# Kernel tuning notes

Hardware: AMD Instinct MI355X
Metric: run time of the kernel (lower is better)

The kernel has to match this reference:

```python
import jax, jax.numpy as jnp
import numpy as np

VOCAB, DIM, HEADS, LAYERS = 32000, 1024, 16, 2
B, S = 2, 1024
HD = DIM // HEADS


def rmsnorm(x, g, eps=1e-6):
    return x * jax.lax.rsqrt(jnp.mean(x * x, axis=-1, keepdims=True) + eps) * g


def setup_inputs() -> dict:
    key = jax.random.key(0)
    ks = jax.random.split(key, 20)
    s = 0.02
    d = {
        "text_ids": jax.random.randint(ks[0], (B, S), 0, VOCAB),
        "embed": jax.random.normal(ks[1], (VOCAB, DIM), jnp.float32) * s,
        "g1": jnp.ones((LAYERS, DIM), jnp.float32),
        "wq": jax.random.normal(ks[2], (LAYERS, DIM, DIM), jnp.float32) * s,
        "bq": jnp.zeros((LAYERS, DIM), jnp.float32),
        "wk": jax.random.normal(ks[3], (LAYERS, DIM, DIM), jnp.float32) * s,
        "bk": jnp.zeros((LAYERS, DIM), jnp.float32),
        "wv": jax.random.normal(ks[4], (LAYERS, DIM, DIM), jnp.float32) * s,
        "bv": jnp.zeros((LAYERS, DIM), jnp.float32),
        "wo": jax.random.normal(ks[5], (LAYERS, DIM, DIM), jnp.float32) * s,
        "bo": jnp.zeros((LAYERS, DIM), jnp.float32),
        "g2": jnp.ones((LAYERS, DIM), jnp.float32),
        "w1": jax.random.normal(ks[6], (LAYERS, DIM, 4 * DIM), jnp.float32) * s,
        "b1": jnp.zeros((LAYERS, 4 * DIM), jnp.float32),
        "w2": jax.random.normal(ks[7], (LAYERS, 4 * DIM, DIM), jnp.float32) * s,
        "b2": jnp.zeros((LAYERS, DIM), jnp.float32),
        "gf": jnp.ones((DIM,), jnp.float32),
        "head_w": jax.random.normal(ks[8], (DIM, VOCAB), jnp.float32) * s,
        "head_b": jnp.zeros((VOCAB,), jnp.float32),
    }
    return d


def reference(text_ids, embed, g1, wq, bq, wk, bk, wv, bv, wo, bo,
              g2, w1, b1, w2, b2, gf, head_w, head_b):
    b, s = text_ids.shape
    x = embed[text_ids]                                   # [B,S,D]
    causal = jnp.tril(jnp.ones((s, s), dtype=bool))        # [S,S]
    scale = 1.0 / jnp.sqrt(jnp.asarray(HD, x.dtype))
    for l in range(LAYERS):
        # attention sublayer: x = x + attn(norm1(x))
        h = rmsnorm(x, g1[l])
        q = (h @ wq[l] + bq[l]).reshape(b, s, HEADS, HD)
        k = (h @ wk[l] + bk[l]).reshape(b, s, HEADS, HD)
        v = (h @ wv[l] + bv[l]).reshape(b, s, HEADS, HD)
        scores = jnp.einsum("bqhd,bkhd->bhqk", q, k) * scale
        scores = jnp.where(causal, scores, jnp.asarray(-1e30, scores.dtype))
        a = jax.nn.softmax(scores, axis=-1)
        o = jnp.einsum("bhqk,bkhd->bqhd", a, v).reshape(b, s, DIM)
        x = x + (o @ wo[l] + bo[l])
        # FFN sublayer: x = x + ffn(norm2(x)), SiLU MLP (MoE unused in source forward)
        h2 = rmsnorm(x, g2[l])
        x = x + (jax.nn.silu(h2 @ w1[l] + b1[l]) @ w2[l] + b2[l])
    x = rmsnorm(x, gf)
    return x.astype(jnp.float32) @ head_w + head_b         # [B,S,VOCAB]
```

## Files before the change

kernel.cpp:

```cpp
#include <hip/hip_runtime.h>

#define LAYERS 2
#define DIM 1024
#define HEADS 16
#define HD 64
#define BATCH 2
#define SEQ 1024
#define ROWS (BATCH * SEQ)
#define FFN (4 * DIM)
#define VOCAB 32000
#define QKVN (3 * DIM)

typedef unsigned short u16;
typedef short vshort8 __attribute__((ext_vector_type(8)));
typedef float f32x4 __attribute__((ext_vector_type(4)));

#define VMCNT(n) asm volatile("s_waitcnt vmcnt(" #n ")" ::: "memory")

__device__ __forceinline__ u16 f2bf(float f) {
  union { float f; unsigned u; } x{f};
  unsigned r = (x.u + 0x7fffu + ((x.u >> 16) & 1u)) >> 16;
  return (u16)r;
}

__device__ __forceinline__ void gll16(const void* g, u16* l) {
  __builtin_amdgcn_global_load_lds(
      (const __attribute__((address_space(1))) void*)g,
      (__attribute__((address_space(3))) void*)l, 16, 0, 0);
}

__device__ __forceinline__ int xcd_swizzle(int orig, int nwg) {
  int q = nwg >> 3, r = nwg & 7;
  int xcd = orig & 7;
  int base = (xcd < r) ? xcd * (q + 1) : r * (q + 1) + (xcd - r) * q;
  return base + (orig >> 3);
}

__global__ __launch_bounds__(256) void transpose_sq_kernel(
    const float* __restrict__ wq, const float* __restrict__ wk,
    const float* __restrict__ wv, const float* __restrict__ wo,
    u16* __restrict__ wqkvT, u16* __restrict__ woT) {
  __shared__ float tile[32][33];
  int z = blockIdx.z, l = z >> 2, wsel = z & 3;
  const float* src =
      (wsel == 0 ? wq : wsel == 1 ? wk : wsel == 2 ? wv : wo) +
      (size_t)l * DIM * DIM;
  u16* dst = (wsel < 3)
                 ? wqkvT + (size_t)l * QKVN * DIM + (size_t)wsel * DIM * DIM
                 : woT + (size_t)l * DIM * DIM;
  int c0 = blockIdx.x * 32, r0 = blockIdx.y * 32;
  int tx = threadIdx.x, ty = threadIdx.y;
#pragma unroll
  for (int i = 0; i < 4; i++)
    tile[ty + i * 8][tx] = src[(size_t)(r0 + ty + i * 8) * DIM + c0 + tx];
  __syncthreads();
#pragma unroll
  for (int i = 0; i < 4; i++)
    dst[(size_t)(c0 + ty + i * 8) * DIM + r0 + tx] = f2bf(tile[tx][ty + i * 8]);
}

template <int R, int C>
__global__ __launch_bounds__(256) void transpose_rc_kernel(
    const float* __restrict__ srcb, u16* __restrict__ dstb) {
  __shared__ float tile[32][33];
  int l = blockIdx.z;
  const float* src = srcb + (size_t)l * R * C;
  u16* dst = dstb + (size_t)l * R * C;
  int c0 = blockIdx.x * 32, r0 = blockIdx.y * 32;
  int tx = threadIdx.x, ty = threadIdx.y;
#pragma unroll
  for (int i = 0; i < 4; i++)
    tile[ty + i * 8][tx] = src[(size_t)(r0 + ty + i * 8) * C + c0 + tx];
  __syncthreads();
#pragma unroll
  for (int i = 0; i < 4; i++)
    dst[(size_t)(c0 + ty + i * 8) * R + r0 + tx] = f2bf(tile[tx][ty + i * 8]);
}

__global__ __launch_bounds__(256) void pack_qkv_bias(
    const float* __restrict__ bq, const float* __restrict__ bk,
    const float* __restrict__ bv, float* __restrict__ o) {
  int l = blockIdx.y;
  int t = blockIdx.x * 256 + threadIdx.x;
  float v;
  if (t < DIM) v = bq[l * DIM + t];
  else if (t < 2 * DIM) v = bk[l * DIM + t - DIM];
  else v = bv[l * DIM + t - 2 * DIM];
  o[(size_t)l * QKVN + t] = v;
}

__global__ __launch_bounds__(256) void embed_gather(
    const int* __restrict__ ids, const float* __restrict__ emb,
    float* __restrict__ x) {
  int row = blockIdx.x;
  int id = ids[row];
  const float4* s = (const float4*)(emb + (size_t)id * DIM);
  float4* d = (float4*)(x + (size_t)row * DIM);
  d[threadIdx.x] = s[threadIdx.x];
}

__global__ __launch_bounds__(256) void rmsnorm_kernel(
    const float* __restrict__ x, const float* __restrict__ g,
    u16* __restrict__ out) {
  int row = blockIdx.x;
  int t = threadIdx.x;
  const float4* xr = (const float4*)(x + (size_t)row * DIM);
  float4 v = xr[t];
  float ss = v.x * v.x + v.y * v.y + v.z * v.z + v.w * v.w;
  for (int off = 32; off > 0; off >>= 1) ss += __shfl_down(ss, off);
  __shared__ float part[4];
  if ((t & 63) == 0) part[t >> 6] = ss;
  __syncthreads();
  float tot = part[0] + part[1] + part[2] + part[3];
  float r = rsqrtf(tot / (float)DIM + 1e-6f);
  float4 gv = ((const float4*)g)[t];
  ushort4 o;
  o.x = f2bf(v.x * r * gv.x);
  o.y = f2bf(v.y * r * gv.y);
  o.z = f2bf(v.z * r * gv.z);
  o.w = f2bf(v.w * r * gv.w);
  *(ushort4*)(out + (size_t)row * DIM + t * 4) = o;
}

__global__ __launch_bounds__(256) void addnorm_kernel(
    float* __restrict__ x, const float* __restrict__ P0,
    const float* __restrict__ P1, const float* __restrict__ bias,
    const float* __restrict__ g, u16* __restrict__ h) {
  int row = blockIdx.x;
  int t = threadIdx.x;
  float4 v = ((const float4*)(x + (size_t)row * DIM))[t];
  float4 a = ((const float4*)(P0 + (size_t)row * DIM))[t];
  float4 b = ((const float4*)(P1 + (size_t)row * DIM))[t];
  float4 c = ((const float4*)bias)[t];
  v.x += a.x + b.x + c.x;
  v.y += a.y + b.y + c.y;
  v.z += a.z + b.z + c.z;
  v.w += a.w + b.w + c.w;
  ((float4*)(x + (size_t)row * DIM))[t] = v;
  float ss = v.x * v.x + v.y * v.y + v.z * v.z + v.w * v.w;
  for (int off = 32; off > 0; off >>= 1) ss += __shfl_down(ss, off);
  __shared__ float part[4];
  if ((t & 63) == 0) part[t >> 6] = ss;
  __syncthreads();
  float tot = part[0] + part[1] + part[2] + part[3];
  float r = rsqrtf(tot / (float)DIM + 1e-6f);
  float4 gv = ((const float4*)g)[t];
  ushort4 o;
  o.x = f2bf(v.x * r * gv.x);
  o.y = f2bf(v.y * r * gv.y);
  o.z = f2bf(v.z * r * gv.z);
  o.w = f2bf(v.w * r * gv.w);
  *(ushort4*)(h + (size_t)row * DIM + t * 4) = o;
}

template <int OUTBF, int SILU, int SPLITK, int MFAST, int VT>
__global__ __launch_bounds__(256, 2) void gemm128_kernel(
    const u16* __restrict__ A, const u16* __restrict__ Wt,
    const float* __restrict__ bias, void* __restrict__ outv,
    float* __restrict__ pout1, u16* __restrict__ vt2, int M, int N, int K) {
  __shared__ u16 As[2][128 * 64];
  __shared__ u16 Bs[2][128 * 64];
  int nm = M >> 7, nn = N >> 7, nwg = nm * nn;
  int wg = xcd_swizzle(blockIdx.x, SPLITK ? nwg * 2 : nwg);
  int ks = 0;
  if (SPLITK) { ks = wg >= nwg; wg -= ks * nwg; }
  int mi, ni;
  if (MFAST) { mi = wg % nm; ni = wg / nm; }
  else       { ni = wg % nn; mi = wg / nn; }
  int m0 = mi << 7, n0 = ni << 7;
  int kb = SPLITK ? ks * (K >> 1) : 0;
  int NTt = (SPLITK ? (K >> 1) : K) >> 6;
  int tid = threadIdx.x, wave = tid >> 6, lane = tid & 63;
  int wr = wave >> 1, wc = wave & 1;
  int r16 = lane & 15, g4 = lane >> 4;
  int lrow = lane >> 3, lslot = lane & 7;

  f32x4 acc[4][4] = {};

  auto stage = [&](int buf, int kt) {
#pragma unroll
    for (int i = 0; i < 4; i++) {
      int s = wave * 4 + i;
      int row = s * 8 + lrow;
      int slot = lslot ^ (row & 7);
      gll16(A + (size_t)(m0 + row) * K + kb + kt * 64 + slot * 8,
            &As[buf][s * 512 + lane * 8]);
    }
#pragma unroll
    for (int i = 0; i < 4; i++) {
      int s = wave * 4 + i;
      int row = s * 8 + lrow;
      int slot = lslot ^ (row & 7);
      gll16(Wt + (size_t)(n0 + row) * K + kb + kt * 64 + slot * 8,
            &Bs[buf][s * 512 + lane * 8]);
    }
  };

  stage(0, 0);
  VMCNT(0);
  __builtin_amdgcn_s_barrier();

  for (int t = 0; t < NTt; t++) {
    int cur = t & 1;
    if (t + 1 < NTt) stage(cur ^ 1, t + 1);
#pragma unroll
    for (int kk = 0; kk < 2; kk++) {
      vshort8 af[4], bf[4];
#pragma unroll
      for (int m = 0; m < 4; m++) {
        int r = wr * 64 + m * 16 + r16;
        int slot = (kk * 4 + g4) ^ (r & 7);
        af[m] = *(const vshort8*)&As[cur][r * 64 + slot * 8];
      }
#pragma unroll
      for (int n = 0; n < 4; n++) {
        int c = wc * 64 + n * 16 + r16;
        int slot = (kk * 4 + g4) ^ (c & 7);
        bf[n] = *(const vshort8*)&Bs[cur][c * 64 + slot * 8];
      }
#pragma unroll
      for (int m = 0; m < 4; m++)
#pragma unroll
        for (int n = 0; n < 4; n++)
          acc[m][n] = __builtin_amdgcn_mfma_f32_16x16x32_bf16(af[m], bf[n],
                                                              acc[m][n], 0, 0, 0);
    }
    VMCNT(0);
    __builtin_amdgcn_s_barrier();
  }

  if (SPLITK) {
    float* P = ks ? pout1 : (float*)outv;
#pragma unroll
    for (int m = 0; m < 4; m++) {
      int rowb = m0 + wr * 64 + m * 16 + g4 * 4;
#pragma unroll
      for (int n = 0; n < 4; n++) {
        int col = n0 + wc * 64 + n * 16 + r16;
#pragma unroll
        for (int j = 0; j < 4; j++)
          P[(size_t)(rowb + j) * N + col] = acc[m][n][j];
      }
    }
  } else {
#pragma unroll
    for (int m = 0; m < 4; m++) {
      int rowb = m0 + wr * 64 + m * 16 + g4 * 4;
#pragma unroll
      for (int n = 0; n < 4; n++) {
        int col = n0 + wc * 64 + n * 16 + r16;
        float b = bias[col];
        u16 ov[4];
#pragma unroll
        for (int j = 0; j < 4; j++) {
          float v = acc[m][n][j] + b;
          if (SILU) v = v / (1.f + __expf(-v));
          if (OUTBF) ov[j] = f2bf(v);
          else ((float*)outv)[(size_t)(rowb + j) * N + col] = v;
        }
        if (OUTBF) {
          if (VT && col >= 2 * DIM) {
            int dv = col - 2 * DIM;
            int hh = dv >> 6, dd = dv & 63;
            int bb = rowb >> 10, s = rowb & 1023;
            ushort4 o4{ov[0], ov[1], ov[2], ov[3]};
            *(ushort4*)&vt2[((((size_t)(bb * 16 + hh) * (SEQ / 8) + (s >> 3)) * 64 +
                              dd) * 8) + (s & 7)] = o4;
          } else {
#pragma unroll
            for (int j = 0; j < 4; j++)
              ((u16*)outv)[(size_t)(rowb + j) * N + col] = ov[j];
          }
        }
      }
    }
  }
}

__global__ __launch_bounds__(512, 2) void gemm256p_kernel(
    const u16* __restrict__ A, const u16* __restrict__ Wt,
    const float* __restrict__ bias, float* __restrict__ out,
    int M, int N, int K) {
  __shared__ u16 As[2][256 * 64];
  __shared__ u16 Bs[2][256 * 64];
  int nn = N >> 8;
  int wg = xcd_swizzle(blockIdx.x, nn * 2);
  int ni = wg >> 1, mhalf = wg & 1;
  int n0 = ni << 8;
  int tid = threadIdx.x, w = tid >> 6, lane = tid & 63;
  int wr = w >> 2, wc = w & 3;
  int r16 = lane & 15, g4 = lane >> 4;
  int srow8 = lane >> 3, sslot = lane & 7;
  const int NTK = 16;
  const int NGT = 64;

  f32x4 acc[8][4] = {};

  auto stageA = [&](int buf, int mb, int kt, int hb, int j) {
    int chunk = j * 8 + w;
    int row = hb * 128 + chunk * 8 + srow8;
    int slot = sslot ^ (row & 7);
    gll16(A + (size_t)(mb + row) * K + kt * 64 + slot * 8,
          &As[buf][hb * 8192 + chunk * 512 + lane * 8]);
  };
  auto stageB = [&](int buf, int kt, int hb, int j) {
    int chunk = j * 8 + w;
    int row = hb * 128 + chunk * 8 + srow8;
    int slot = sslot ^ (row & 7);
    gll16(Wt + (size_t)(n0 + row) * K + kt * 64 + slot * 8,
          &Bs[buf][hb * 8192 + chunk * 512 + lane * 8]);
  };
  auto readA = [&](int buf, int mf, int kk) -> vshort8 {
    int row = mf * 32 + wr * 16 + r16;
    int slot = (kk * 4 + g4) ^ (row & 7);
    return *(const vshort8*)&As[buf][row * 64 + slot * 8];
  };
  auto readB = [&](int buf, int nf, int kk) -> vshort8 {
    int row = nf * 64 + wc * 16 + r16;
    int slot = (kk * 4 + g4) ^ (row & 7);
    return *(const vshort8*)&Bs[buf][row * 64 + slot * 8];
  };

  int mb0 = (mhalf * 4) << 8;
  stageA(0, mb0, 0, 0, 0); stageA(0, mb0, 0, 0, 1);
  stageB(0, 0, 0, 0);      stageB(0, 0, 0, 1);
  stageB(0, 0, 1, 0);      stageB(0, 0, 1, 1);
  stageA(0, mb0, 0, 1, 0); stageA(0, mb0, 0, 1, 1);
  VMCNT(2);
  __builtin_amdgcn_s_barrier();

  vshort8 af[4][2], bf0[2][2], bf1[2][2];

  for (int ti = 0; ti < 4; ti++) {
    int m0 = (mhalf * 4 + ti) << 8;
    for (int tt = 0; tt < NTK; tt++) {
      int gt = ti * NTK + tt;
      int cur = gt & 1, nxt = cur ^ 1;
      int gt1 = gt + 1;
      bool hn = gt1 < NGT;
      int kt1 = gt1 & (NTK - 1);
      int mb1 = (mhalf * 4 + (gt1 >> 4)) << 8;
      if (hn) {
        stageA(nxt, mb1, kt1, 0, 0); stageA(nxt, mb1, kt1, 0, 1);
        stageB(nxt, kt1, 0, 0);      stageB(nxt, kt1, 0, 1);
        stageB(nxt, kt1, 1, 0);      stageB(nxt, kt1, 1, 1);
      }
#pragma unroll
      for (int m = 0; m < 4; m++)
#pragma unroll
        for (int kk = 0; kk < 2; kk++) af[m][kk] = readA(cur, m, kk);
#pragma unroll
      for (int n = 0; n < 2; n++)
#pragma unroll
        for (int kk = 0; kk < 2; kk++) {
          bf0[n][kk] = readB(cur, n, kk);
          bf1[n][kk] = readB(cur, 2 + n, kk);
        }
      __builtin_amdgcn_s_barrier();
      __builtin_amdgcn_s_setprio(1);
#pragma unroll
      for (int m = 0; m < 4; m++)
#pragma unroll
        for (int n = 0; n < 2; n++)
#pragma unroll
          for (int kk = 0; kk < 2; kk++) {
            acc[m][n] = __builtin_amdgcn_mfma_f32_16x16x32_bf16(
                af[m][kk], bf0[n][kk], acc[m][n], 0, 0, 0);
            acc[m][n + 2] = __builtin_amdgcn_mfma_f32_16x16x32_bf16(
                af[m][kk], bf1[n][kk], acc[m][n + 2], 0, 0, 0);
          }
      __builtin_amdgcn_s_setprio(0);
      VMCNT(6);
      __builtin_amdgcn_s_barrier();
      if (hn) { stageA(nxt, mb1, kt1, 1, 0); stageA(nxt, mb1, kt1, 1, 1); }
#pragma unroll
      for (int m = 0; m < 4; m++)
#pragma unroll
        for (int kk = 0; kk < 2; kk++) af[m][kk] = readA(cur, 4 + m, kk);
      __builtin_amdgcn_s_barrier();
      __builtin_amdgcn_s_setprio(1);
#pragma unroll
      for (int m = 0; m < 4; m++)
#pragma unroll
        for (int n = 0; n < 2; n++)
#pragma unroll
          for (int kk = 0; kk < 2; kk++) {
            acc[m + 4][n] = __builtin_amdgcn_mfma_f32_16x16x32_bf16(
                af[m][kk], bf0[n][kk], acc[m + 4][n], 0, 0, 0);
            acc[m + 4][n + 2] = __builtin_amdgcn_mfma_f32_16x16x32_bf16(
                af[m][kk], bf1[n][kk], acc[m + 4][n + 2], 0, 0, 0);
          }
      __builtin_amdgcn_s_setprio(0);
      VMCNT(2);
      __builtin_amdgcn_s_barrier();
    }
#pragma unroll
    for (int mf = 0; mf < 8; mf++) {
      int rowb = m0 + mf * 32 + wr * 16 + g4 * 4;
#pragma unroll
      for (int nf = 0; nf < 4; nf++) {
        int col = n0 + nf * 64 + wc * 16 + r16;
        float b = bias[col];
#pragma unroll
        for (int j = 0; j < 4; j++)
          out[(size_t)(rowb + j) * N + col] = acc[mf][nf][j] + b;
      }
    }
#pragma unroll
    for (int mf = 0; mf < 8; mf++)
#pragma unroll
      for (int nf = 0; nf < 4; nf++) acc[mf][nf] = f32x4{0.f, 0.f, 0.f, 0.f};
  }
}

__global__ __launch_bounds__(256) void attn_kernel(const u16* __restrict__ qkv,
                                                   const u16* __restrict__ vt2,
                                                   u16* __restrict__ o) {
  __shared__ u16 Ks[2][32 * 64];
  __shared__ u16 pl[4][16 * 40];
  int qblk = blockIdx.x, bh = blockIdx.y;
  int b = bh >> 4, h = bh & 15;
  int tid = threadIdx.x, w = tid >> 6, lane = tid & 63;
  int r16 = lane & 15, g4 = lane >> 4;
  int q0 = qblk * 64 + w * 16;

  const u16* qrow = qkv + ((size_t)(b * SEQ) + q0 + r16) * QKVN + h * HD;
  vshort8 aq0 = *(const vshort8*)(qrow + g4 * 8);
  vshort8 aq1 = *(const vshort8*)(qrow + 32 + g4 * 8);

  float mrun[4], lrun[4];
  f32x4 accO[4];
#pragma unroll
  for (int j = 0; j < 4; j++) { mrun[j] = -1e30f; lrun[j] = 0.f; }
#pragma unroll
  for (int d = 0; d < 4; d++) accO[d] = f32x4{0.f, 0.f, 0.f, 0.f};

  int nkvT = qblk * 2 + 2;
  auto stageK = [&](int buf, int kt) {
    int row = tid >> 3;
    int slot = (tid & 7) ^ (row & 7);
    gll16(qkv + ((size_t)(b * SEQ) + kt * 32 + row) * QKVN + DIM + h * HD + slot * 8,
          &Ks[buf][w * 512 + lane * 8]);
  };
  stageK(0, 0);
  __syncthreads();
  int buf = 0;
  for (int kt = 0; kt < nkvT; kt++) {
    int kv0 = kt * 32;
    if (kt + 1 < nkvT) stageK(buf ^ 1, kt + 1);
    if (kv0 <= q0 + 15) {
      int row0 = r16, row1 = 16 + r16;
      vshort8 bk00 = *(const vshort8*)&Ks[buf][row0 * 64 + ((0 + g4) ^ (row0 & 7)) * 8];
      vshort8 bk01 = *(const vshort8*)&Ks[buf][row0 * 64 + ((4 + g4) ^ (row0 & 7)) * 8];
      vshort8 bk10 = *(const vshort8*)&Ks[buf][row1 * 64 + ((0 + g4) ^ (row1 & 7)) * 8];
      vshort8 bk11 = *(const vshort8*)&Ks[buf][row1 * 64 + ((4 + g4) ^ (row1 & 7)) * 8];
      f32x4 s0 = {}, s1 = {};
      s0 = __builtin_amdgcn_mfma_f32_16x16x32_bf16(aq0, bk00, s0, 0, 0, 0);
      s0 = __builtin_amdgcn_mfma_f32_16x16x32_bf16(aq1, bk01, s0, 0, 0, 0);
      s1 = __builtin_amdgcn_mfma_f32_16x16x32_bf16(aq0, bk10, s1, 0, 0, 0);
      s1 = __builtin_amdgcn_mfma_f32_16x16x32_bf16(aq1, bk11, s1, 0, 0, 0);

#pragma unroll
      for (int j = 0; j < 4; j++) {
        int qg = q0 + g4 * 4 + j;
        float x0 = s0[j] * 0.125f;
        float x1 = s1[j] * 0.125f;
        if (kv0 + r16 > qg) x0 = -1e30f;
        if (kv0 + 16 + r16 > qg) x1 = -1e30f;
        float mx = fmaxf(x0, x1);
#pragma unroll
        for (int mm = 1; mm < 16; mm <<= 1) mx = fmaxf(mx, __shfl_xor(mx, mm));
        float mnew = fmaxf(mrun[j], mx);
        float alpha = __expf(mrun[j] - mnew);
        float p0 = __expf(x0 - mnew);
        float p1 = __expf(x1 - mnew);
        float rs = p0 + p1;
#pragma unroll
        for (int mm = 1; mm < 16; mm <<= 1) rs += __shfl_xor(rs, mm);
        lrun[j] = lrun[j] * alpha + rs;
        mrun[j] = mnew;
#pragma unroll
        for (int d = 0; d < 4; d++) accO[d][j] *= alpha;
        pl[w][(g4 * 4 + j) * 40 + r16] = f2bf(p0);
        pl[w][(g4 * 4 + j) * 40 + 16 + r16] = f2bf(p1);
      }
      asm volatile("s_waitcnt lgkmcnt(0)" ::: "memory");
      vshort8 ap = *(const vshort8*)&pl[w][r16 * 40 + g4 * 8];
      const u16* vbase = vt2 + (((size_t)bh * (SEQ / 8) + (kv0 >> 3) + g4) * 64) * 8;
#pragma unroll
      for (int d = 0; d < 4; d++) {
        vshort8 bv = *(const vshort8*)(vbase + (size_t)(d * 16 + r16) * 8);
        accO[d] = __builtin_amdgcn_mfma_f32_16x16x32_bf16(ap, bv, accO[d], 0, 0, 0);
      }
    }
    __syncthreads();
    buf ^= 1;
  }

#pragma unroll
  for (int j = 0; j < 4; j++) {
    float inv = 1.f / lrun[j];
    int row = q0 + g4 * 4 + j;
#pragma unroll
    for (int d = 0; d < 4; d++)
      o[((size_t)(b * SEQ) + row) * DIM + h * HD + d * 16 + r16] =
          f2bf(accO[d][j] * inv);
  }
}

extern "C" void kernel_launch(void* const* d_in, const int* in_sizes, int n_in,
                              void* d_out, int out_size, void* d_ws,
                              size_t ws_size, hipStream_t stream) {
  const int* ids = (const int*)d_in[0];
  const float* emb = (const float*)d_in[1];
  const float* g1 = (const float*)d_in[2];
  const float* wq = (const float*)d_in[3];
  const float* bq = (const float*)d_in[4];
  const float* wk = (const float*)d_in[5];
  const float* bk = (const float*)d_in[6];
  const float* wv = (const float*)d_in[7];
  const float* bv = (const float*)d_in[8];
  const float* wo = (const float*)d_in[9];
  const float* bo = (const float*)d_in[10];
  const float* g2 = (const float*)d_in[11];
  const float* w1 = (const float*)d_in[12];
  const float* b1 = (const float*)d_in[13];
  const float* w2 = (const float*)d_in[14];
  const float* b2 = (const float*)d_in[15];
  const float* gf = (const float*)d_in[16];
  const float* head_w = (const float*)d_in[17];
  const float* head_b = (const float*)d_in[18];
  float* out = (float*)d_out;

  char* ws = (char*)d_ws;
  size_t off = 0;
  auto alloc = [&](size_t bytes) -> char* {
    char* p = ws + off;
    off += (bytes + 255) & ~(size_t)255;
    return p;
  };
  u16* wqkvT = (u16*)alloc((size_t)LAYERS * QKVN * DIM * 2);
  u16* woT = (u16*)alloc((size_t)LAYERS * DIM * DIM * 2);
  u16* w1T = (u16*)alloc((size_t)LAYERS * DIM * FFN * 2);
  u16* w2T = (u16*)alloc((size_t)LAYERS * DIM * FFN * 2);
  u16* headT = (u16*)alloc((size_t)VOCAB * DIM * 2);
  float* bqkv = (float*)alloc((size_t)LAYERS * QKVN * 4);
  float* x = (float*)alloc((size_t)ROWS * DIM * 4);
  u16* h = (u16*)alloc((size_t)ROWS * DIM * 2);
  u16* qkvb = (u16*)alloc((size_t)ROWS * QKVN * 2);
  u16* vtb = (u16*)alloc((size_t)ROWS * DIM * 2);
  u16* ob = (u16*)alloc((size_t)ROWS * DIM * 2);
  u16* tb = (u16*)alloc((size_t)ROWS * FFN * 2);
  float* P0 = (float*)alloc((size_t)ROWS * DIM * 4);
  float* P1 = (float*)alloc((size_t)ROWS * DIM * 4);
  if (off > ws_size) return;

  dim3 tb32(32, 8);
  transpose_sq_kernel<<<dim3(DIM / 32, DIM / 32, 4 * LAYERS), tb32, 0, stream>>>(
      wq, wk, wv, wo, wqkvT, woT);
  transpose_rc_kernel<DIM, FFN>
      <<<dim3(FFN / 32, DIM / 32, LAYERS), tb32, 0, stream>>>(w1, w1T);
  transpose_rc_kernel<FFN, DIM>
      <<<dim3(DIM / 32, FFN / 32, LAYERS), tb32, 0, stream>>>(w2, w2T);
  transpose_rc_kernel<DIM, VOCAB>
      <<<dim3(VOCAB / 32, DIM / 32, 1), tb32, 0, stream>>>(head_w, headT);
  pack_qkv_bias<<<dim3(QKVN / 256, LAYERS), 256, 0, stream>>>(bq, bk, bv, bqkv);

  embed_gather<<<ROWS, 256, 0, stream>>>(ids, emb, x);
  rmsnorm_kernel<<<ROWS, 256, 0, stream>>>(x, g1, h);

  for (int l = 0; l < LAYERS; l++) {
    gemm128_kernel<1, 0, 0, 1, 1>
        <<<(ROWS / 128) * (QKVN / 128), 256, 0, stream>>>(
            h, wqkvT + (size_t)l * QKVN * DIM, bqkv + (size_t)l * QKVN,
            qkvb, nullptr, vtb, ROWS, QKVN, DIM);
    attn_kernel<<<dim3(SEQ / 64, BATCH * HEADS), 256, 0, stream>>>(qkvb, vtb, ob);
    gemm128_kernel<0, 0, 1, 0, 0>
        <<<2 * (ROWS / 128) * (DIM / 128), 256, 0, stream>>>(
            ob, woT + (size_t)l * DIM * DIM, nullptr, P0, P1, nullptr,
            ROWS, DIM, DIM);
    addnorm_kernel<<<ROWS, 256, 0, stream>>>(
        x, P0, P1, bo + (size_t)l * DIM, g2 + (size_t)l * DIM, h);
    gemm128_kernel<1, 1, 0, 1, 0>
        <<<(ROWS / 128) * (FFN / 128), 256, 0, stream>>>(
            h, w1T + (size_t)l * DIM * FFN, b1 + (size_t)l * FFN, tb, nullptr,
            nullptr, ROWS, FFN, DIM);
    gemm128_kernel<0, 0, 1, 0, 0>
        <<<2 * (ROWS / 128) * (DIM / 128), 256, 0, stream>>>(
            tb, w2T + (size_t)l * DIM * FFN, nullptr, P0, P1, nullptr,
            ROWS, DIM, FFN);
    addnorm_kernel<<<ROWS, 256, 0, stream>>>(
        x, P0, P1, b2 + (size_t)l * DIM,
        (l == LAYERS - 1) ? gf : (g1 + (size_t)(l + 1) * DIM), h);
  }
  gemm256p_kernel<<<(VOCAB / 256) * 2, 512, 0, stream>>>(
      h, headT, head_b, out, ROWS, VOCAB, DIM);
}
```

Before: 658.4 us.

## Fuse embed gather with rmsnorm and restage head GEMM into four phases

Merges the embedding gather and the first rmsnorm into one kernel, which removes a launch and a round trip of the activation through memory. The big (likely LM-head) GEMM main loop is split into four MFMA phases, each interleaved with a slice of the next tile's global-to-LDS staging, so loads are spread more evenly across compute. This adds extra barriers per k-step and a full vmcnt(0) wait in the prologue, and the wait counts must match the new staging order to stay correct.

```diff
diff --git a/kernel.cpp b/kernel.cpp
--- a/kernel.cpp
+++ b/kernel.cpp
@@ -89,23 +89,14 @@
   o[(size_t)l * QKVN + t] = v;
 }
 
-__global__ __launch_bounds__(256) void embed_gather(
+__global__ __launch_bounds__(256) void embed_norm_kernel(
     const int* __restrict__ ids, const float* __restrict__ emb,
-    float* __restrict__ x) {
-  int row = blockIdx.x;
-  int id = ids[row];
-  const float4* s = (const float4*)(emb + (size_t)id * DIM);
-  float4* d = (float4*)(x + (size_t)row * DIM);
-  d[threadIdx.x] = s[threadIdx.x];
-}
-
-__global__ __launch_bounds__(256) void rmsnorm_kernel(
-    const float* __restrict__ x, const float* __restrict__ g,
-    u16* __restrict__ out) {
+    const float* __restrict__ g, float* __restrict__ x, u16* __restrict__ h) {
   int row = blockIdx.x;
   int t = threadIdx.x;
-  const float4* xr = (const float4*)(x + (size_t)row * DIM);
-  float4 v = xr[t];
+  int id = ids[row];
+  float4 v = ((const float4*)(emb + (size_t)id * DIM))[t];
+  ((float4*)(x + (size_t)row * DIM))[t] = v;
   float ss = v.x * v.x + v.y * v.y + v.z * v.z + v.w * v.w;
   for (int off = 32; off > 0; off >>= 1) ss += __shfl_down(ss, off);
   __shared__ float part[4];
@@ -119,7 +110,7 @@
   o.y = f2bf(v.y * r * gv.y);
   o.z = f2bf(v.z * r * gv.z);
   o.w = f2bf(v.w * r * gv.w);
-  *(ushort4*)(out + (size_t)row * DIM + t * 4) = o;
+  *(ushort4*)(h + (size_t)row * DIM + t * 4) = o;
 }
 
 __global__ __launch_bounds__(256) void addnorm_kernel(
@@ -326,7 +317,7 @@
   stageB(0, 0, 0, 0);      stageB(0, 0, 0, 1);
   stageB(0, 0, 1, 0);      stageB(0, 0, 1, 1);
   stageA(0, mb0, 0, 1, 0); stageA(0, mb0, 0, 1, 1);
-  VMCNT(2);
+  VMCNT(0);
   __builtin_amdgcn_s_barrier();
 
   vshort8 af[4][2], bf0[2][2], bf1[2][2];
@@ -340,11 +331,6 @@
       bool hn = gt1 < NGT;
       int kt1 = gt1 & (NTK - 1);
       int mb1 = (mhalf * 4 + (gt1 >> 4)) << 8;
-      if (hn) {
-        stageA(nxt, mb1, kt1, 0, 0); stageA(nxt, mb1, kt1, 0, 1);
-        stageB(nxt, kt1, 0, 0);      stageB(nxt, kt1, 0, 1);
-        stageB(nxt, kt1, 1, 0);      stageB(nxt, kt1, 1, 1);
-      }
 #pragma unroll
       for (int m = 0; m < 4; m++)
 #pragma unroll
@@ -352,10 +338,8 @@
 #pragma unroll
       for (int n = 0; n < 2; n++)
 #pragma unroll
-        for (int kk = 0; kk < 2; kk++) {
-          bf0[n][kk] = readB(cur, n, kk);
-          bf1[n][kk] = readB(cur, 2 + n, kk);
-        }
+        for (int kk = 0; kk < 2; kk++) bf0[n][kk] = readB(cur, n, kk);
+      if (hn) { stageA(nxt, mb1, kt1, 0, 0); stageA(nxt, mb1, kt1, 0, 1); }
       __builtin_amdgcn_s_barrier();
       __builtin_amdgcn_s_setprio(1);
 #pragma unroll
@@ -363,35 +347,61 @@
 #pragma unroll
         for (int n = 0; n < 2; n++)
 #pragma unroll
-          for (int kk = 0; kk < 2; kk++) {
+          for (int kk = 0; kk < 2; kk++)
             acc[m][n] = __builtin_amdgcn_mfma_f32_16x16x32_bf16(
                 af[m][kk], bf0[n][kk], acc[m][n], 0, 0, 0);
+      __builtin_amdgcn_s_setprio(0);
+      VMCNT(4);
+      __builtin_amdgcn_s_barrier();
+#pragma unroll
+      for (int n = 0; n < 2; n++)
+#pragma unroll
+        for (int kk = 0; kk < 2; kk++) bf1[n][kk] = readB(cur, 2 + n, kk);
+      if (hn) { stageB(nxt, kt1, 0, 0); stageB(nxt, kt1, 0, 1); }
+      __builtin_amdgcn_s_barrier();
+      __builtin_amdgcn_s_setprio(1);
+#pragma unroll
+      for (int m = 0; m < 4; m++)
+#pragma unroll
+        for (int n = 0; n < 2; n++)
+#pragma unroll
+          for (int kk = 0; kk < 2; kk++)
             acc[m][n + 2] = __builtin_amdgcn_mfma_f32_16x16x32_bf16(
                 af[m][kk], bf1[n][kk], acc[m][n + 2], 0, 0, 0);
-          }
       __builtin_amdgcn_s_setprio(0);
-      VMCNT(6);
+      VMCNT(4);
+      __builtin_amdgcn_s_barrier();
+#pragma unroll
+      for (int m = 0; m < 4; m++)
+#pragma unroll
+        for (int kk = 0; kk < 2; kk++) af[m][kk] = readA(cur, 4 + m, kk);
+      if (hn) { stageB(nxt, kt1, 1, 0); stageB(nxt, kt1, 1, 1); }
+      __builtin_amdgcn_s_barrier();
+      __builtin_amdgcn_s_setprio(1);
+#pragma unroll
+      for (int m = 0; m < 4; m++)
+#pragma unroll
+        for (int n = 0; n < 2; n++)
+#pragma unroll
+          for (int kk = 0; kk < 2; kk++)
+            acc[m + 4][n + 2] = __builtin_amdgcn_mfma_f32_16x16x32_bf16(
+                af[m][kk], bf1[n][kk], acc[m + 4][n + 2], 0, 0, 0);
+      __builtin_amdgcn_s_setprio(0);
+      VMCNT(4);
       __builtin_amdgcn_s_barrier();
       if (hn) { stageA(nxt, mb1, kt1, 1, 0); stageA(nxt, mb1, kt1, 1, 1); }
+      __builtin_amdgcn_s_barrier();
+      __builtin_amdgcn_s_setprio(1);
 #pragma unroll
       for (int m = 0; m < 4; m++)
 #pragma unroll
-        for (int kk = 0; kk < 2; kk++) af[m][kk] = readA(cur, 4 + m, kk);
-      __builtin_amdgcn_s_barrier();
-      __builtin_amdgcn_s_setprio(1);
-#pragma unroll
-      for (int m = 0; m < 4; m++)
-#pragma unroll
         for (int n = 0; n < 2; n++)
 #pragma unroll
-          for (int kk = 0; kk < 2; kk++) {
+          for (int kk = 0; kk < 2; kk++)
             acc[m + 4][n] = __builtin_amdgcn_mfma_f32_16x16x32_bf16(
                 af[m][kk], bf0[n][kk], acc[m + 4][n], 0, 0, 0);
-            acc[m + 4][n + 2] = __builtin_amdgcn_mfma_f32_16x16x32_bf16(
-                af[m][kk], bf1[n][kk], acc[m + 4][n + 2], 0, 0, 0);
-          }
       __builtin_amdgcn_s_setprio(0);
-      VMCNT(2);
+      VMCNT(4);
       __builtin_amdgcn_s_barrier();
     }
 #pragma unroll
@@ -566,8 +576,7 @@
       <<<dim3(VOCAB / 32, DIM / 32, 1), tb32, 0, stream>>>(head_w, headT);
   pack_qkv_bias<<<dim3(QKVN / 256, LAYERS), 256, 0, stream>>>(bq, bk, bv, bqkv);
 
-  embed_gather<<<ROWS, 256, 0, stream>>>(ids, emb, x);
-  rmsnorm_kernel<<<ROWS, 256, 0, stream>>>(x, g1, h);
+  embed_norm_kernel<<<ROWS, 256, 0, stream>>>(ids, emb, g1, x, h);
 
   for (int l = 0; l < LAYERS; l++) {
     gemm128_kernel<1, 0, 0, 1, 1>
```

Result: faster. 605.2 us (-8.1%).
